# Performance work log

Hardware: AMD Instinct MI355X
Metric: run time of the kernel (lower is better)

Reference implementation:

```python
import jax, jax.numpy as jnp
import numpy as np

H = W = 32          # gussin() is hard-coded to width=32 in BASE
C = 512             # BASE inner_nc; down conv is 1024->512
V = 1.5             # gaussian sigma


def _gaussian_weights():
    # Vectorized equivalent of gussin(1.5): g[p, x, y] for p = i*W + k,
    # g = exp(-((x-i)^2+(y-k)^2)/(2 v^2)) / (2 pi v^2), normalized per p.
    idx = np.arange(H, dtype=np.float64)
    d1 = (idx[:, None] - idx[None, :]) ** 2            # (i, x)
    d2 = d1[:, None, :, None] + d1[None, :, None, :]    # (i, k, x, y)
    g = np.exp(-d2 / (2.0 * V * V)) / (2.0 * np.pi * V * V)
    g = g.reshape(H * W, H, W)
    g = g / g.sum(axis=(1, 2), keepdims=True)
    return jnp.asarray(g, dtype=jnp.float32)


def _instance_norm(x, eps=1e-5):
    # InstanceNorm2d(affine=False): per-(b,c) mean/biased-var over (h,w)
    mu = x.mean(axis=(2, 3), keepdims=True)
    var = jnp.mean((x - mu) ** 2, axis=(2, 3), keepdims=True)
    return (x - mu) / jnp.sqrt(var + eps)


def _patches3(fm):
    # fm: (C, H+2, W+2) zero-padded map -> 3x3 patches: (H*W, C, 3, 3)
    p = jnp.stack([fm[:, di:di + H, dj:dj + W]
                   for di in range(3) for dj in range(3)], axis=-1)  # (C,H,W,9)
    return p.transpose(1, 2, 0, 3).reshape(H * W, C, 3, 3)


def setup_inputs() -> dict:
    key = jax.random.key(0)
    ks = jax.random.split(key, 4)
    x = jax.random.normal(ks[0], (1, C, H, W), jnp.float32)
    w_se1 = jax.random.normal(ks[1], (C // 16, C), jnp.float32) * 0.05   # SE squeeze fc
    w_se2 = jax.random.normal(ks[2], (C, C // 16), jnp.float32) * 0.05   # SE excite fc
    w_down = jax.random.normal(ks[3], (C, 2 * C, 1, 1), jnp.float32) * 0.05  # 1x1 conv 1024->512
    return {"x": x, "w_se1": w_se1, "w_se2": w_se2, "w_down": w_down}


def reference(x, w_se1, w_se2, w_down):
    gus = _gaussian_weights()                                # (HW, H, W), constant
    # --- SELayer(512, 16) ---
    s = x.mean(axis=(2, 3))                                  # (1, C) global avg pool
    s = jax.nn.relu(s @ w_se1.T)                             # (1, C/16)
    s = jax.nn.sigmoid(s @ w_se2.T)                          # (1, C)
    out32 = x * s[:, :, None, None]                          # (1, C, H, W)
    # --- gaussian-weighted pooling (einsum instead of (HW,C,H,W) broadcast) ---
    gus_out = jnp.einsum('pxy,cxy->pc', gus, out32[0])       # (HW, C)
    gus_out = gus_out.reshape(1, C, H, W)                    # raw reshape, as in torch .view
    # --- patch-based contextual self-attention (CSA) ---
    sig = jax.nn.sigmoid(out32)                              # (1, C, H, W)
    sig_pad = jnp.pad(sig[0], ((0, 0), (1, 1), (1, 1)))
    raw_pad = jnp.pad(out32[0], ((0, 0), (1, 1), (1, 1)))
    p_sig = _patches3(sig_pad)                               # (HW, C, 3, 3)
    p_raw = _patches3(raw_pad)                               # (HW, C, 3, 3)
    center = sig[0].transpose(1, 2, 0).reshape(H * W, C, 1, 1)  # center sigmoid vec per loc
    score = jnp.mean(center * p_sig, axis=1)                 # (HW, 3, 3)
    attn = jax.nn.softmax(score.reshape(H * W, 9), axis=1).reshape(H * W, 1, 3, 3)
    out_csa = jnp.sum(attn * p_raw, axis=(2, 3))             # (HW, C)
    out_csa = out_csa.reshape(1, C, H, W)                    # raw reshape, as in torch .view
    # --- concat + 1x1 conv down + InstanceNorm + LeakyReLU(0.2) ---
    cat = jnp.concatenate([gus_out, out_csa], axis=1)        # (1, 2C, H, W)
    y = jnp.einsum('bihw,oi->bohw', cat, w_down[:, :, 0, 0])
    y = _instance_norm(y)
    return jnp.where(y >= 0, y, 0.2 * y)
```

## Files before the change

kernel.cpp:

```cpp
#include <hip/hip_runtime.h>


__device__ __forceinline__ float block_reduce_256(float v, float* sm4) {
  #pragma unroll
  for (int off = 32; off >= 1; off >>= 1) v += __shfl_down(v, off);
  __syncthreads();
  if ((threadIdx.x & 63) == 0) sm4[threadIdx.x >> 6] = v;
  __syncthreads();
  return sm4[0] + sm4[1] + sm4[2] + sm4[3];
}

__global__ void k_mean_gn(const float* __restrict__ x, float* __restrict__ smean,
                          float* __restrict__ gn) {
  if (blockIdx.x == 512) {
    int tid = threadIdx.x;
    int a = tid >> 3;
    int b0 = (tid & 7) * 4;
    float e[4];
    float s = 0.0f;
    #pragma unroll
    for (int q = 0; q < 4; q++) {
      float d = (float)(a - (b0 + q));
      e[q] = __expf(d * d * (-1.0f / 4.5f));
      s += e[q];
    }
    s += __shfl_xor(s, 1, 8);
    s += __shfl_xor(s, 2, 8);
    s += __shfl_xor(s, 4, 8);
    float inv = 1.0f / s;
    #pragma unroll
    for (int q = 0; q < 4; q++) gn[a * 32 + b0 + q] = e[q] * inv;
    return;
  }
  __shared__ float sm4[4];
  int c = blockIdx.x;
  const float* row = x + c * 1024;
  float s = 0.0f;
  for (int i = threadIdx.x; i < 1024; i += 256) s += row[i];
  float t = block_reduce_256(s, sm4);
  if (threadIdx.x == 0) smean[c] = t * (1.0f / 1024.0f);
}

__global__ void k_apply(const float* __restrict__ x, const float* __restrict__ smean,
                        const float* __restrict__ w1, const float* __restrict__ w2,
                        float* __restrict__ out32, float* __restrict__ out32T,
                        float* __restrict__ sigT) {
  __shared__ float sm[512];
  __shared__ float s1[32];
  __shared__ float sc[32];
  __shared__ float tile[32][33];
  int tid = threadIdx.x;
  for (int i = tid; i < 512; i += 256) sm[i] = smean[i];
  __syncthreads();
  int j = tid >> 3, l8 = tid & 7;
  float a = 0.0f;
  for (int cc = l8; cc < 512; cc += 8) a += sm[cc] * w1[j * 512 + cc];
  a += __shfl_down(a, 4, 8);
  a += __shfl_down(a, 2, 8);
  a += __shfl_down(a, 1, 8);
  if (l8 == 0) s1[j] = fmaxf(a, 0.0f);
  __syncthreads();
  int c0 = blockIdx.y * 32, hw0 = blockIdx.x * 32;
  if (tid < 32) {
    float b = 0.0f;
    #pragma unroll
    for (int jj = 0; jj < 32; jj++) b += s1[jj] * w2[(c0 + tid) * 32 + jj];
    sc[tid] = 1.0f / (1.0f + __expf(-b));
  }
  __syncthreads();
  int tx = tid & 31, ty = tid >> 5;
  #pragma unroll
  for (int r = 0; r < 4; r++) {
    int c = ty + 8 * r;
    float v = x[(c0 + c) * 1024 + hw0 + tx] * sc[c];
    out32[(c0 + c) * 1024 + hw0 + tx] = v;
    tile[c][tx] = v;
  }
  __syncthreads();
  #pragma unroll
  for (int r = 0; r < 4; r++) {
    int hw = ty + 8 * r;
    float v = tile[tx][hw];
    out32T[(hw0 + hw) * 512 + c0 + tx] = v;
    sigT[(hw0 + hw) * 512 + c0 + tx] = 1.0f / (1.0f + __expf(-v));
  }
}

__global__ void k_gausscsa(const float* __restrict__ out32, const float* __restrict__ gn,
                           const float* __restrict__ sigT, const float* __restrict__ out32T,
                           float* __restrict__ catg) {
  if (blockIdx.x < 512) {
    __shared__ float row[32 * 33];
    __shared__ float g[1024];
    __shared__ float tt[32 * 33];
    int c = blockIdx.x;
    int tid = threadIdx.x;
    for (int idx = tid; idx < 1024; idx += 256) {
      row[(idx >> 5) * 33 + (idx & 31)] = out32[c * 1024 + idx];
      g[idx] = gn[idx];
    }
    __syncthreads();
    for (int idx = tid; idx < 1024; idx += 256) {
      int k = idx >> 5, xx = idx & 31;
      float s = 0.0f;
      #pragma unroll
      for (int y = 0; y < 32; y++) s += g[k * 32 + y] * row[xx * 33 + y];
      tt[k * 33 + xx] = s;
    }
    __syncthreads();
    for (int p = tid; p < 1024; p += 256) {
      int i = p >> 5, k = p & 31;
      float s = 0.0f;
      #pragma unroll
      for (int x = 0; x < 32; x++) s += g[i * 32 + x] * tt[k * 33 + x];
      catg[p * 512 + c] = s;
    }
  } else {
    int wv = threadIdx.x >> 6;
    int lane = threadIdx.x & 63;
    int p = (blockIdx.x - 512) * 4 + wv;
    int h = p >> 5, w = p & 31;
    int c0 = lane * 8;
    float4 ce0 = *(const float4*)&sigT[p * 512 + c0];
    float4 ce1 = *(const float4*)&sigT[p * 512 + c0 + 4];
    int qoff[9];
    float s[9];
    #pragma unroll
    for (int dd = 0; dd < 9; dd++) {
      int hh = h + dd / 3 - 1, ww = w + (dd % 3) - 1;
      bool v = (hh >= 0) && (hh < 32) && (ww >= 0) && (ww < 32);
      qoff[dd] = v ? (hh * 32 + ww) * 512 : -1;
      float a = 0.0f;
      if (v) {
        float4 n0 = *(const float4*)&sigT[qoff[dd] + c0];
        float4 n1 = *(const float4*)&sigT[qoff[dd] + c0 + 4];
        a = ce0.x * n0.x + ce0.y * n0.y + ce0.z * n0.z + ce0.w * n0.w
          + ce1.x * n1.x + ce1.y * n1.y + ce1.z * n1.z + ce1.w * n1.w;
      }
      #pragma unroll
      for (int off = 32; off >= 1; off >>= 1) a += __shfl_xor(a, off);
      s[dd] = a;
    }
    float mx = -1e30f;
    #pragma unroll
    for (int dd = 0; dd < 9; dd++) { s[dd] *= (1.0f / 512.0f); mx = fmaxf(mx, s[dd]); }
    float tot = 0.0f;
    #pragma unroll
    for (int dd = 0; dd < 9; dd++) { s[dd] = __expf(s[dd] - mx); tot += s[dd]; }
    float inv = 1.0f / tot;
    float4 o0 = make_float4(0, 0, 0, 0), o1 = make_float4(0, 0, 0, 0);
    #pragma unroll
    for (int dd = 0; dd < 9; dd++) {
      if (qoff[dd] >= 0) {
        float att = s[dd] * inv;
        float4 r0 = *(const float4*)&out32T[qoff[dd] + c0];
        float4 r1 = *(const float4*)&out32T[qoff[dd] + c0 + 4];
        o0.x += att * r0.x; o0.y += att * r0.y; o0.z += att * r0.z; o0.w += att * r0.w;
        o1.x += att * r1.x; o1.y += att * r1.y; o1.z += att * r1.z; o1.w += att * r1.w;
      }
    }
    *(float4*)&catg[524288 + p * 512 + c0] = o0;
    *(float4*)&catg[524288 + p * 512 + c0 + 4] = o1;
  }
}

__global__ void k_gemm(const float* __restrict__ A, const float* __restrict__ B,
                       float* __restrict__ Cp) {
  __shared__ __align__(16) float As[32][68];
  __shared__ __align__(16) float Bs[32][64];
  int tid = threadIdx.x;
  int tx = tid & 15;
  int ty = tid >> 4;
  int bn = blockIdx.x * 64;
  int bm = blockIdx.y * 64;
  int zK = blockIdx.z * 128;
  int a_m = tid >> 5;
  int a_k = tid & 31;
  int b_row = tid >> 4;
  int b_q = tid & 15;
  float acc[4][4] = {};
  for (int k0 = 0; k0 < 128; k0 += 32) {
    #pragma unroll
    for (int r = 0; r < 8; r++) {
      As[a_k][a_m + 8 * r] = A[(bm + a_m + 8 * r) * 1024 + zK + k0 + a_k];
    }
    #pragma unroll
    for (int r = 0; r < 2; r++) {
      float4 v = *(const float4*)&B[(zK + k0 + b_row + 16 * r) * 1024 + bn + b_q * 4];
      *(float4*)&Bs[b_row + 16 * r][b_q * 4] = v;
    }
    __syncthreads();
    #pragma unroll
    for (int k = 0; k < 32; k++) {
      float4 av = *(const float4*)&As[k][ty * 4];
      float4 bv = *(const float4*)&Bs[k][tx * 4];
      acc[0][0] += av.x * bv.x; acc[0][1] += av.x * bv.y; acc[0][2] += av.x * bv.z; acc[0][3] += av.x * bv.w;
      acc[1][0] += av.y * bv.x; acc[1][1] += av.y * bv.y; acc[1][2] += av.y * bv.z; acc[1][3] += av.y * bv.w;
      acc[2][0] += av.z * bv.x; acc[2][1] += av.z * bv.y; acc[2][2] += av.z * bv.z; acc[2][3] += av.z * bv.w;
      acc[3][0] += av.w * bv.x; acc[3][1] += av.w * bv.y; acc[3][2] += av.w * bv.z; acc[3][3] += av.w * bv.w;
    }
    __syncthreads();
  }
  float* Cz = Cp + blockIdx.z * 524288;
  #pragma unroll
  for (int i = 0; i < 4; i++) {
    float4 v = make_float4(acc[i][0], acc[i][1], acc[i][2], acc[i][3]);
    *(float4*)&Cz[(bm + ty * 4 + i) * 1024 + bn + tx * 4] = v;
  }
}

__global__ void k_inorm(const float* __restrict__ yp, float* __restrict__ out) {
  __shared__ float sm4[4];
  __shared__ float vrow[1024];
  int o = blockIdx.x;
  const float* r0 = yp + o * 1024;
  float s = 0.0f, q = 0.0f;
  for (int i = threadIdx.x; i < 1024; i += 256) {
    float v = 0.0f;
    #pragma unroll
    for (int j = 0; j < 8; j++) v += r0[i + j * 524288];
    vrow[i] = v;
    s += v; q += v * v;
  }
  float ts = block_reduce_256(s, sm4);
  float tq = block_reduce_256(q, sm4);
  float mean = ts * (1.0f / 1024.0f);
  float var = tq * (1.0f / 1024.0f) - mean * mean;
  float inv = rsqrtf(var + 1e-5f);
  for (int i = threadIdx.x; i < 1024; i += 256) {
    float v = (vrow[i] - mean) * inv;
    out[o * 1024 + i] = v >= 0.0f ? v : 0.2f * v;
  }
}

extern "C" void kernel_launch(void* const* d_in, const int* in_sizes, int n_in,
                              void* d_out, int out_size, void* d_ws, size_t ws_size,
                              hipStream_t stream) {
  const float* x      = (const float*)d_in[0];
  const float* w_se1  = (const float*)d_in[1];
  const float* w_se2  = (const float*)d_in[2];
  const float* w_down = (const float*)d_in[3];
  float* out = (float*)d_out;

  float* ws = (float*)d_ws;
  float* gn     = ws;
  float* smean  = ws + 1024;
  float* out32  = ws + 2048;
  float* out32T = out32 + 524288;
  float* sigT   = out32T + 524288;
  float* cat    = sigT + 524288;
  float* ypart  = cat + 1048576;

  k_mean_gn<<<513, 256, 0, stream>>>(x, smean, gn);
  k_apply<<<dim3(32, 16), 256, 0, stream>>>(x, smean, w_se1, w_se2, out32, out32T, sigT);
  k_gausscsa<<<768, 256, 0, stream>>>(out32, gn, sigT, out32T, cat);
  k_gemm<<<dim3(16, 8, 8), 256, 0, stream>>>(w_down, cat, ypart);
  k_inorm<<<512, 256, 0, stream>>>(ypart, out);
}
```

Before: 117.2 us.

## Use bf16 MFMA for down-projection GEMM and split gaussian pooling into coalesced passes

Replaces the fp32 SIMT split-K GEMM with a bf16 MFMA 16x16x32 kernel. The weights and the concatenated activations are converted to bf16 and the activations are stored transposed, K-major. The gaussian separable pooling is split into two channel-coalesced kernels (k_g1csa, k_g2) working on a swizzled channel-last copy, and they write bf16 directly into the GEMM operand layout. The split-K partial sums drop from 8 to 2, which cuts instance-norm reads. This adds a kernel launch and a T1 intermediate, and bf16 rounding reduces accuracy. The CSA branch now writes scattered 2-byte stores.

```diff
diff --git a/kernel.cpp b/kernel.cpp
--- a/kernel.cpp
+++ b/kernel.cpp
@@ -1,6 +1,17 @@
 #include <hip/hip_runtime.h>
 
 
+typedef short short8 __attribute__((ext_vector_type(8)));
+typedef short short4v __attribute__((ext_vector_type(4)));
+typedef float floatx4 __attribute__((ext_vector_type(4)));
+
+__device__ __forceinline__ unsigned short f2bf(float x) {
+  union { float f; unsigned u; } v; v.f = x;
+  unsigned u = v.u;
+  u = (u + 0x7fffu + ((u >> 16) & 1u)) >> 16;
+  return (unsigned short)u;
+}
+
 __device__ __forceinline__ float block_reduce_256(float v, float* sm4) {
   #pragma unroll
   for (int off = 32; off >= 1; off >>= 1) v += __shfl_down(v, off);
@@ -11,7 +22,18 @@
 }
 
 __global__ void k_mean_gn(const float* __restrict__ x, float* __restrict__ smean,
-                          float* __restrict__ gn) {
+                          float* __restrict__ gn, const float* __restrict__ wdn,
+                          unsigned short* __restrict__ Abf) {
+  if (blockIdx.x > 512) {
+    int base = (blockIdx.x - 513) * 2048 + threadIdx.x * 8;
+    float4 a = *(const float4*)&wdn[base];
+    float4 b = *(const float4*)&wdn[base + 4];
+    short8 s;
+    s[0] = (short)f2bf(a.x); s[1] = (short)f2bf(a.y); s[2] = (short)f2bf(a.z); s[3] = (short)f2bf(a.w);
+    s[4] = (short)f2bf(b.x); s[5] = (short)f2bf(b.y); s[6] = (short)f2bf(b.z); s[7] = (short)f2bf(b.w);
+    *(short8*)&Abf[base] = s;
+    return;
+  }
   if (blockIdx.x == 512) {
     int tid = threadIdx.x;
     int a = tid >> 3;
@@ -43,8 +65,8 @@
 
 __global__ void k_apply(const float* __restrict__ x, const float* __restrict__ smean,
                         const float* __restrict__ w1, const float* __restrict__ w2,
-                        float* __restrict__ out32, float* __restrict__ out32T,
-                        float* __restrict__ sigT) {
+                        float* __restrict__ out32T, float* __restrict__ sigT,
+                        float* __restrict__ V) {
   __shared__ float sm[512];
   __shared__ float s1[32];
   __shared__ float sc[32];
@@ -73,48 +95,48 @@
   for (int r = 0; r < 4; r++) {
     int c = ty + 8 * r;
     float v = x[(c0 + c) * 1024 + hw0 + tx] * sc[c];
-    out32[(c0 + c) * 1024 + hw0 + tx] = v;
     tile[c][tx] = v;
   }
   __syncthreads();
   #pragma unroll
   for (int r = 0; r < 4; r++) {
-    int hw = ty + 8 * r;
-    float v = tile[tx][hw];
-    out32T[(hw0 + hw) * 512 + c0 + tx] = v;
-    sigT[(hw0 + hw) * 512 + c0 + tx] = 1.0f / (1.0f + __expf(-v));
-  }
-}
-
-__global__ void k_gausscsa(const float* __restrict__ out32, const float* __restrict__ gn,
-                           const float* __restrict__ sigT, const float* __restrict__ out32T,
-                           float* __restrict__ catg) {
+    int hw = hw0 + ty + 8 * r;
+    float v = tile[tx][ty + 8 * r];
+    out32T[hw * 512 + c0 + tx] = v;
+    sigT[hw * 512 + c0 + tx] = 1.0f / (1.0f + __expf(-v));
+    int hwsw = ((hw & 31) << 5) | (hw >> 5);
+    V[hwsw * 512 + c0 + tx] = v;
+  }
+}
+
+__global__ void k_g1csa(const float* __restrict__ V, const float* __restrict__ gn,
+                        const float* __restrict__ sigT, const float* __restrict__ out32T,
+                        float* __restrict__ T1, unsigned short* __restrict__ catT) {
   if (blockIdx.x < 512) {
-    __shared__ float row[32 * 33];
     __shared__ float g[1024];
-    __shared__ float tt[32 * 33];
-    int c = blockIdx.x;
     int tid = threadIdx.x;
-    for (int idx = tid; idx < 1024; idx += 256) {
-      row[(idx >> 5) * 33 + (idx & 31)] = out32[c * 1024 + idx];
-      g[idx] = gn[idx];
-    }
+    for (int i = tid; i < 1024; i += 256) g[i] = gn[i];
     __syncthreads();
-    for (int idx = tid; idx < 1024; idx += 256) {
-      int k = idx >> 5, xx = idx & 31;
-      float s = 0.0f;
-      #pragma unroll
-      for (int y = 0; y < 32; y++) s += g[k * 32 + y] * row[xx * 33 + y];
-      tt[k * 33 + xx] = s;
-    }
-    __syncthreads();
-    for (int p = tid; p < 1024; p += 256) {
-      int i = p >> 5, k = p & 31;
-      float s = 0.0f;
-      #pragma unroll
-      for (int x = 0; x < 32; x++) s += g[i * 32 + x] * tt[k * 33 + x];
-      catg[p * 512 + c] = s;
-    }
+    int t = blockIdx.x * 256 + tid;
+    int c = t & 511;
+    int xk = t >> 9;
+    int xx = xk & 31, kg = xk >> 5;
+    const float* vp = V + xx * 512 + c;
+    const float* g0 = g + kg * 4 * 32;
+    float s0 = 0, s1 = 0, s2 = 0, s3 = 0;
+    #pragma unroll 8
+    for (int y = 0; y < 32; y++) {
+      float vv = vp[y * 16384];
+      s0 += g0[y] * vv;
+      s1 += g0[32 + y] * vv;
+      s2 += g0[64 + y] * vv;
+      s3 += g0[96 + y] * vv;
+    }
+    int ko = kg * 4 * 32 + xx;
+    T1[ko * 512 + c] = s0;
+    T1[(ko + 32) * 512 + c] = s1;
+    T1[(ko + 64) * 512 + c] = s2;
+    T1[(ko + 96) * 512 + c] = s3;
   } else {
     int wv = threadIdx.x >> 6;
     int lane = threadIdx.x & 63;
@@ -148,64 +170,80 @@
     #pragma unroll
     for (int dd = 0; dd < 9; dd++) { s[dd] = __expf(s[dd] - mx); tot += s[dd]; }
     float inv = 1.0f / tot;
-    float4 o0 = make_float4(0, 0, 0, 0), o1 = make_float4(0, 0, 0, 0);
+    float o[8] = {0, 0, 0, 0, 0, 0, 0, 0};
     #pragma unroll
     for (int dd = 0; dd < 9; dd++) {
       if (qoff[dd] >= 0) {
         float att = s[dd] * inv;
         float4 r0 = *(const float4*)&out32T[qoff[dd] + c0];
         float4 r1 = *(const float4*)&out32T[qoff[dd] + c0 + 4];
-        o0.x += att * r0.x; o0.y += att * r0.y; o0.z += att * r0.z; o0.w += att * r0.w;
-        o1.x += att * r1.x; o1.y += att * r1.y; o1.z += att * r1.z; o1.w += att * r1.w;
+        o[0] += att * r0.x; o[1] += att * r0.y; o[2] += att * r0.z; o[3] += att * r0.w;
+        o[4] += att * r1.x; o[5] += att * r1.y; o[6] += att * r1.z; o[7] += att * r1.w;
       }
     }
-    *(float4*)&catg[524288 + p * 512 + c0] = o0;
-    *(float4*)&catg[524288 + p * 512 + c0 + 4] = o1;
-  }
-}
-
-__global__ void k_gemm(const float* __restrict__ A, const float* __restrict__ B,
-                       float* __restrict__ Cp) {
-  __shared__ __align__(16) float As[32][68];
-  __shared__ __align__(16) float Bs[32][64];
+    int kcol = 512 + (p >> 1);
+    int nbase = (p & 1) * 512 + c0;
+    #pragma unroll
+    for (int q = 0; q < 8; q++) catT[(nbase + q) * 1024 + kcol] = f2bf(o[q]);
+  }
+}
+
+__global__ void k_g2(const float* __restrict__ T1, const float* __restrict__ gn,
+                     unsigned short* __restrict__ catT) {
+  __shared__ float g[1024];
   int tid = threadIdx.x;
-  int tx = tid & 15;
-  int ty = tid >> 4;
-  int bn = blockIdx.x * 64;
-  int bm = blockIdx.y * 64;
-  int zK = blockIdx.z * 128;
-  int a_m = tid >> 5;
-  int a_k = tid & 31;
-  int b_row = tid >> 4;
-  int b_q = tid & 15;
-  float acc[4][4] = {};
-  for (int k0 = 0; k0 < 128; k0 += 32) {
-    #pragma unroll
-    for (int r = 0; r < 8; r++) {
-      As[a_k][a_m + 8 * r] = A[(bm + a_m + 8 * r) * 1024 + zK + k0 + a_k];
-    }
-    #pragma unroll
-    for (int r = 0; r < 2; r++) {
-      float4 v = *(const float4*)&B[(zK + k0 + b_row + 16 * r) * 1024 + bn + b_q * 4];
-      *(float4*)&Bs[b_row + 16 * r][b_q * 4] = v;
-    }
-    __syncthreads();
-    #pragma unroll
-    for (int k = 0; k < 32; k++) {
-      float4 av = *(const float4*)&As[k][ty * 4];
-      float4 bv = *(const float4*)&Bs[k][tx * 4];
-      acc[0][0] += av.x * bv.x; acc[0][1] += av.x * bv.y; acc[0][2] += av.x * bv.z; acc[0][3] += av.x * bv.w;
-      acc[1][0] += av.y * bv.x; acc[1][1] += av.y * bv.y; acc[1][2] += av.y * bv.z; acc[1][3] += av.y * bv.w;
-      acc[2][0] += av.z * bv.x; acc[2][1] += av.z * bv.y; acc[2][2] += av.z * bv.z; acc[2][3] += av.z * bv.w;
-      acc[3][0] += av.w * bv.x; acc[3][1] += av.w * bv.y; acc[3][2] += av.w * bv.z; acc[3][3] += av.w * bv.w;
-    }
-    __syncthreads();
-  }
-  float* Cz = Cp + blockIdx.z * 524288;
-  #pragma unroll
-  for (int i = 0; i < 4; i++) {
-    float4 v = make_float4(acc[i][0], acc[i][1], acc[i][2], acc[i][3]);
-    *(float4*)&Cz[(bm + ty * 4 + i) * 1024 + bn + tx * 4] = v;
+  for (int i = tid; i < 1024; i += 256) g[i] = gn[i];
+  __syncthreads();
+  int t = blockIdx.x * 256 + tid;
+  int c = t & 511;
+  int rest = t >> 9;
+  int i = rest >> 3;
+  int sub = rest & 7;
+  int par = sub & 1, kq = sub >> 1;
+  const float* tp = T1 + c;
+  const float* gi = g + i * 32;
+  float s0 = 0, s1 = 0, s2 = 0, s3 = 0;
+  int kb = kq * 8 + par;
+  #pragma unroll 8
+  for (int xx = 0; xx < 32; xx++) {
+    float gv = gi[xx];
+    s0 += gv * tp[((kb + 0) * 32 + xx) * 512];
+    s1 += gv * tp[((kb + 2) * 32 + xx) * 512];
+    s2 += gv * tp[((kb + 4) * 32 + xx) * 512];
+    s3 += gv * tp[((kb + 6) * 32 + xx) * 512];
+  }
+  short4v o;
+  o[0] = (short)f2bf(s0); o[1] = (short)f2bf(s1); o[2] = (short)f2bf(s2); o[3] = (short)f2bf(s3);
+  *(short4v*)&catT[(par * 512 + c) * 1024 + i * 16 + kq * 4] = o;
+}
+
+__global__ void k_gemm(const unsigned short* __restrict__ Abf,
+                       const unsigned short* __restrict__ Bbf,
+                       float* __restrict__ yp) {
+  int wv = threadIdx.x >> 6, lane = threadIdx.x & 63;
+  int w0 = blockIdx.x;
+  int m = w0 >> 4;
+  int n0 = (w0 & 15) * 64;
+  int nn = n0 + (wv & 1) * 32;
+  int kz = wv >> 1;
+  int l16 = lane & 15, quad = lane >> 4;
+  const short8* ap  = (const short8*)(Abf + (m * 16 + l16) * 1024 + kz * 512 + quad * 8);
+  const short8* bp0 = (const short8*)(Bbf + (nn + l16) * 1024 + kz * 512 + quad * 8);
+  const short8* bp1 = (const short8*)(Bbf + (nn + 16 + l16) * 1024 + kz * 512 + quad * 8);
+  floatx4 acc0 = {0.f, 0.f, 0.f, 0.f}, acc1 = {0.f, 0.f, 0.f, 0.f};
+  #pragma unroll 4
+  for (int kk = 0; kk < 16; kk++) {
+    short8 a  = ap[kk * 4];
+    short8 b0 = bp0[kk * 4];
+    short8 b1 = bp1[kk * 4];
+    acc0 = __builtin_amdgcn_mfma_f32_16x16x32_bf16(a, b0, acc0, 0, 0, 0);
+    acc1 = __builtin_amdgcn_mfma_f32_16x16x32_bf16(a, b1, acc1, 0, 0, 0);
+  }
+  float* yo = yp + kz * 524288 + (m * 16 + quad * 4) * 1024 + l16;
+  #pragma unroll
+  for (int r = 0; r < 4; r++) {
+    yo[r * 1024 + nn] = acc0[r];
+    yo[r * 1024 + nn + 16] = acc1[r];
   }
 }
 
@@ -216,9 +254,7 @@
   const float* r0 = yp + o * 1024;
   float s = 0.0f, q = 0.0f;
   for (int i = threadIdx.x; i < 1024; i += 256) {
-    float v = 0.0f;
-    #pragma unroll
-    for (int j = 0; j < 8; j++) v += r0[i + j * 524288];
+    float v = r0[i] + r0[i + 524288];
     vrow[i] = v;
     s += v; q += v * v;
   }
@@ -245,15 +281,18 @@
   float* ws = (float*)d_ws;
   float* gn     = ws;
   float* smean  = ws + 1024;
-  float* out32  = ws + 2048;
-  float* out32T = out32 + 524288;
+  float* out32T = ws + 2048;
   float* sigT   = out32T + 524288;
-  float* cat    = sigT + 524288;
-  float* ypart  = cat + 1048576;
-
-  k_mean_gn<<<513, 256, 0, stream>>>(x, smean, gn);
-  k_apply<<<dim3(32, 16), 256, 0, stream>>>(x, smean, w_se1, w_se2, out32, out32T, sigT);
-  k_gausscsa<<<768, 256, 0, stream>>>(out32, gn, sigT, out32T, cat);
-  k_gemm<<<dim3(16, 8, 8), 256, 0, stream>>>(w_down, cat, ypart);
-  k_inorm<<<512, 256, 0, stream>>>(ypart, out);
-}
+  float* V      = sigT + 524288;
+  float* T1     = V + 524288;
+  unsigned short* catT = (unsigned short*)(T1 + 524288);
+  unsigned short* Abf  = (unsigned short*)(T1 + 1048576);
+  float* yp     = T1 + 1310720;
+
+  k_mean_gn<<<769, 256, 0, stream>>>(x, smean, gn, w_down, Abf);
+  k_apply<<<dim3(32, 16), 256, 0, stream>>>(x, smean, w_se1, w_se2, out32T, sigT, V);
+  k_g1csa<<<768, 256, 0, stream>>>(V, gn, sigT, out32T, T1, catT);
+  k_g2<<<512, 256, 0, stream>>>(T1, gn, catT);
+  k_gemm<<<512, 256, 0, stream>>>(Abf, catT, yp);
+  k_inorm<<<512, 256, 0, stream>>>(yp, out);
+}
```

Result: faster. 111.7 us (-4.7%).
